# Performance work log

Measured on AMD Instinct MI355X. Metric: run time of the kernel, lower is better.

The kernel has to match this reference:

```python
import jax, jax.numpy as jnp
import numpy as np

H = 12          # trees_num / n_heads
D_WEIGHT = 0.1  # opt['d_weight']
NEG = -1e9


def setup_inputs() -> dict:
    key = jax.random.key(0)
    ks = jax.random.split(key, 6)
    B, N, D = 8, 512, 768
    inp = {}
    inp["input"] = jax.random.normal(ks[0], (B, N, D), dtype=jnp.float32)
    inp["src_mask"] = jax.random.randint(ks[1], (B, 1, N), 0, 2).astype(jnp.int32)
    inp["dep_emb"] = jax.random.normal(ks[2], (B, N, N), dtype=jnp.float32)
    s = 1.0 / np.sqrt(D)
    inp["Wq"] = jax.random.normal(ks[3], (D, D), dtype=jnp.float32) * s
    inp["bq"] = jnp.zeros((D,), dtype=jnp.float32)
    inp["Wk"] = jax.random.normal(ks[4], (D, D), dtype=jnp.float32) * s
    inp["bk"] = jnp.zeros((D,), dtype=jnp.float32)
    return inp


def reference(input, src_mask, dep_emb, Wq, bq, Wk, bk):
    B, N, D = input.shape
    dk = D // H
    # Q/K projections -> [B, H, N, dk]
    q = (input @ Wq + bq).reshape(B, N, H, dk).transpose(0, 2, 1, 3)
    k = (input @ Wk + bk).reshape(B, N, H, dk).transpose(0, 2, 1, 3)
    # scaled scores [B, H, N, N]
    scores = jnp.einsum("bhqd,bhkd->bhqk", q, k) / jnp.sqrt(jnp.asarray(dk, input.dtype))
    # blend with dependency bias: dep_emb [B,N,N] -> [B,1,N,N]
    scores = (1.0 - D_WEIGHT) * scores + D_WEIGHT * dep_emb[:, None, :, :]
    # mask: src_mask [B,1,N] -> [B,1,1,N]; masked_fill(mask==0, -1e9)
    scores = jnp.where(src_mask[:, None, :, :] == 0, NEG, scores)
    p_attn = jax.nn.softmax(scores, axis=-1)  # [B, H, N, N]
    # original returns list of per-head [B,N,N]; full tensor is equivalent
    return p_attn
```

## Files before the change

### kernel.cpp

```cpp
#include <hip/hip_runtime.h>


typedef _Float16 f16;
typedef _Float16 f16x4 __attribute__((ext_vector_type(4)));
typedef _Float16 f16x8 __attribute__((ext_vector_type(8)));
typedef float    f32x4 __attribute__((ext_vector_type(4)));

#define NTOK   512
#define DMODEL 768
#define BATCH  8
#define NHEAD  12
#define NEGV   (-1e9f)

__global__ __launch_bounds__(256)
void convert_x(const float* __restrict__ X, f16* __restrict__ Xh) {
    const size_t i = ((size_t)blockIdx.x * 256 + threadIdx.x) * 4;
    float4 v = *(const float4*)&X[i];
    f16x4 h = { (f16)v.x, (f16)v.y, (f16)v.z, (f16)v.w };
    *(f16x4*)&Xh[i] = h;
}

__global__ __launch_bounds__(256)
void transpose_w(const float* __restrict__ Wq, const float* __restrict__ Wk,
                 f16* __restrict__ Wt) {
    __shared__ float tile[32][33];
    const int kb = blockIdx.x * 32;
    const int nb = blockIdx.y * 32;
    const float* __restrict__ W = (nb < 768) ? Wq : Wk;
    const int nc = (nb < 768) ? nb : nb - 768;
    const int tx = threadIdx.x, ty = threadIdx.y;
    #pragma unroll
    for (int i = 0; i < 4; ++i)
        tile[ty + i*8][tx] = W[(size_t)(kb + ty + i*8) * DMODEL + nc + tx];
    __syncthreads();
    #pragma unroll
    for (int i = 0; i < 4; ++i)
        Wt[(size_t)(nb + ty + i*8) * DMODEL + kb + tx] = (f16)tile[tx][ty + i*8];
}

__global__ __launch_bounds__(64)
void proj_mfma(const f16* __restrict__ Xh, const f16* __restrict__ Wt,
               const float* __restrict__ bq, const float* __restrict__ bk,
               f16* __restrict__ QK) {
    const int m0 = blockIdx.x * 64;
    const int n0 = blockIdx.y * 64;
    const int l = threadIdx.x;
    const int l15 = l & 15, quad = l >> 4;

    f32x4 acc[4][4];
    #pragma unroll
    for (int i = 0; i < 4; ++i)
        #pragma unroll
        for (int j = 0; j < 4; ++j) acc[i][j] = (f32x4){0.f, 0.f, 0.f, 0.f};

    const f16* __restrict__ Ab = Xh + (size_t)(m0 + l15) * DMODEL + quad * 8;
    const f16* __restrict__ Bb = Wt + (size_t)(n0 + l15) * DMODEL + quad * 8;

    for (int ks = 0; ks < DMODEL / 32; ++ks) {
        f16x8 a[4], b[4];
        #pragma unroll
        for (int mi = 0; mi < 4; ++mi)
            a[mi] = *(const f16x8*)(Ab + (size_t)mi * 16 * DMODEL + ks * 32);
        #pragma unroll
        for (int ni = 0; ni < 4; ++ni)
            b[ni] = *(const f16x8*)(Bb + (size_t)ni * 16 * DMODEL + ks * 32);
        #pragma unroll
        for (int mi = 0; mi < 4; ++mi)
            #pragma unroll
            for (int ni = 0; ni < 4; ++ni)
                acc[mi][ni] = __builtin_amdgcn_mfma_f32_16x16x32_f16(
                    a[mi], b[ni], acc[mi][ni], 0, 0, 0);
    }

    const float* __restrict__ bias = (n0 < 768) ? (bq + n0) : (bk + n0 - 768);
    #pragma unroll
    for (int ni = 0; ni < 4; ++ni) {
        const float bv = bias[ni * 16 + l15];
        const int col = n0 + ni * 16 + l15;
        #pragma unroll
        for (int mi = 0; mi < 4; ++mi) {
            #pragma unroll
            for (int r = 0; r < 4; ++r) {
                const int row = m0 + mi * 16 + quad * 4 + r;
                QK[(size_t)row * 1536 + col] = (f16)(acc[mi][ni][r] + bv);
            }
        }
    }
}

__global__ __launch_bounds__(64)
void attn_mfma(const f16* __restrict__ QK, const float* __restrict__ dep,
               const int* __restrict__ mask, float* __restrict__ out) {
    const int qt = blockIdx.x, h = blockIdx.y, b = blockIdx.z;
    const int l = threadIdx.x;
    const int l15 = l & 15, quad = l >> 4;
    const int q0 = qt * 16;

    f32x4 acc[32];
    #pragma unroll
    for (int t = 0; t < 32; ++t) acc[t] = (f32x4){0.f, 0.f, 0.f, 0.f};

    const f16* __restrict__ Qb = QK + (size_t)(b * NTOK + q0 + l15) * 1536 + h * 64 + quad * 8;
    const f16* __restrict__ Kb = QK + (size_t)(b * NTOK + l15) * 1536 + 768 + h * 64 + quad * 8;

    #pragma unroll
    for (int ks = 0; ks < 2; ++ks) {
        f16x8 a = *(const f16x8*)(Qb + ks * 32);
        #pragma unroll
        for (int t = 0; t < 32; ++t) {
            f16x8 bf = *(const f16x8*)(Kb + (size_t)t * 16 * 1536 + ks * 32);
            acc[t] = __builtin_amdgcn_mfma_f32_16x16x32_f16(a, bf, acc[t], 0, 0, 0);
        }
    }

    const float SC = (1.0f - 0.1f) / 8.0f;
    const float DW = 0.1f;
    const float* __restrict__ deprow = dep + ((size_t)b * NTOK + q0 + quad * 4) * NTOK;
    const int*   __restrict__ mrow   = mask + b * NTOK;
    #pragma unroll
    for (int t = 0; t < 32; ++t) {
        const int col = t * 16 + l15;
        const int mv = mrow[col];
        #pragma unroll
        for (int r = 0; r < 4; ++r) {
            const float dv = deprow[(size_t)r * NTOK + col];
            const float s = SC * acc[t][r] + DW * dv;
            acc[t][r] = mv ? s : NEGV;
        }
    }

    float rmax[4] = {NEGV, NEGV, NEGV, NEGV};
    #pragma unroll
    for (int t = 0; t < 32; ++t)
        #pragma unroll
        for (int r = 0; r < 4; ++r) rmax[r] = fmaxf(rmax[r], acc[t][r]);
    #pragma unroll
    for (int r = 0; r < 4; ++r) {
        rmax[r] = fmaxf(rmax[r], __shfl_xor(rmax[r], 1));
        rmax[r] = fmaxf(rmax[r], __shfl_xor(rmax[r], 2));
        rmax[r] = fmaxf(rmax[r], __shfl_xor(rmax[r], 4));
        rmax[r] = fmaxf(rmax[r], __shfl_xor(rmax[r], 8));
    }
    float rsum[4] = {0.f, 0.f, 0.f, 0.f};
    #pragma unroll
    for (int t = 0; t < 32; ++t)
        #pragma unroll
        for (int r = 0; r < 4; ++r) {
            const float e = __expf(acc[t][r] - rmax[r]);
            acc[t][r] = e;
            rsum[r] += e;
        }
    #pragma unroll
    for (int r = 0; r < 4; ++r) {
        rsum[r] += __shfl_xor(rsum[r], 1);
        rsum[r] += __shfl_xor(rsum[r], 2);
        rsum[r] += __shfl_xor(rsum[r], 4);
        rsum[r] += __shfl_xor(rsum[r], 8);
    }
    float inv[4];
    #pragma unroll
    for (int r = 0; r < 4; ++r) inv[r] = 1.0f / rsum[r];

    float* __restrict__ orow = out + ((size_t)((b * NHEAD + h) * NTOK) + q0 + quad * 4) * NTOK;
    #pragma unroll
    for (int t = 0; t < 32; ++t)
        #pragma unroll
        for (int r = 0; r < 4; ++r)
            orow[(size_t)r * NTOK + t * 16 + l15] = acc[t][r] * inv[r];
}

extern "C" void kernel_launch(void* const* d_in, const int* in_sizes, int n_in,
                              void* d_out, int out_size, void* d_ws, size_t ws_size,
                              hipStream_t stream) {
    const float* X    = (const float*)d_in[0];
    const int*   mask = (const int*)  d_in[1];
    const float* dep  = (const float*)d_in[2];
    const float* Wq   = (const float*)d_in[3];
    const float* bq   = (const float*)d_in[4];
    const float* Wk   = (const float*)d_in[5];
    const float* bk   = (const float*)d_in[6];
    float* out = (float*)d_out;

    f16* Xh = (f16*)d_ws;
    f16* Wt = Xh + (size_t)BATCH * NTOK * DMODEL;
    f16* QK = Wt + (size_t)1536 * DMODEL;

    convert_x<<<dim3((BATCH * NTOK * DMODEL) / (256 * 4)), 256, 0, stream>>>(X, Xh);
    transpose_w<<<dim3(DMODEL / 32, 1536 / 32), dim3(32, 8), 0, stream>>>(Wq, Wk, Wt);
    proj_mfma<<<dim3((BATCH * NTOK) / 64, 1536 / 64), 64, 0, stream>>>(Xh, Wt, bq, bk, QK);
    attn_mfma<<<dim3(NTOK / 16, NHEAD, BATCH), 64, 0, stream>>>(QK, dep, mask, out);
}
```

Before: 206.9 us.

## Stage per-head K tile in LDS shared by four waves; merge prep kernels

The attention kernel now uses 256-thread blocks covering 64 query rows. Each block loads the head's full K slice (512x64 f16, padded rows) into shared memory once, and all four waves reuse it, so K is no longer re-read from global memory for every 16-row tile. Separately, the X conversion and weight transpose are merged into one launch to save a kernel launch. The cost is a 72KB LDS allocation per block, which limits occupancy, plus a barrier before any compute can start.

```diff
diff --git a/kernel.cpp b/kernel.cpp
--- a/kernel.cpp
+++ b/kernel.cpp
@@ -11,31 +11,34 @@
 #define BATCH  8
 #define NHEAD  12
 #define NEGV   (-1e9f)
+#define KPAD   72
 
 __global__ __launch_bounds__(256)
-void convert_x(const float* __restrict__ X, f16* __restrict__ Xh) {
-    const size_t i = ((size_t)blockIdx.x * 256 + threadIdx.x) * 4;
-    float4 v = *(const float4*)&X[i];
-    f16x4 h = { (f16)v.x, (f16)v.y, (f16)v.z, (f16)v.w };
-    *(f16x4*)&Xh[i] = h;
-}
-
-__global__ __launch_bounds__(256)
-void transpose_w(const float* __restrict__ Wq, const float* __restrict__ Wk,
+void prep_kernel(const float* __restrict__ X, f16* __restrict__ Xh,
+                 const float* __restrict__ Wq, const float* __restrict__ Wk,
                  f16* __restrict__ Wt) {
-    __shared__ float tile[32][33];
-    const int kb = blockIdx.x * 32;
-    const int nb = blockIdx.y * 32;
-    const float* __restrict__ W = (nb < 768) ? Wq : Wk;
-    const int nc = (nb < 768) ? nb : nb - 768;
-    const int tx = threadIdx.x, ty = threadIdx.y;
-    #pragma unroll
-    for (int i = 0; i < 4; ++i)
-        tile[ty + i*8][tx] = W[(size_t)(kb + ty + i*8) * DMODEL + nc + tx];
-    __syncthreads();
-    #pragma unroll
-    for (int i = 0; i < 4; ++i)
-        Wt[(size_t)(nb + ty + i*8) * DMODEL + kb + tx] = (f16)tile[tx][ty + i*8];
+    const int bx = blockIdx.x;
+    if (bx < 3072) {
+        const size_t i = ((size_t)bx * 256 + threadIdx.x) * 4;
+        float4 v = *(const float4*)&X[i];
+        f16x4 h = { (f16)v.x, (f16)v.y, (f16)v.z, (f16)v.w };
+        *(f16x4*)&Xh[i] = h;
+    } else {
+        __shared__ float tile[32][33];
+        const int id = bx - 3072;
+        const int kb = (id % 24) * 32;
+        const int nb = (id / 24) * 32;
+        const float* __restrict__ W = (nb < 768) ? Wq : Wk;
+        const int nc = (nb < 768) ? nb : nb - 768;
+        const int tx = threadIdx.x & 31, ty = threadIdx.x >> 5;
+        #pragma unroll
+        for (int i = 0; i < 4; ++i)
+            tile[ty + i*8][tx] = W[(size_t)(kb + ty + i*8) * DMODEL + nc + tx];
+        __syncthreads();
+        #pragma unroll
+        for (int i = 0; i < 4; ++i)
+            Wt[(size_t)(nb + ty + i*8) * DMODEL + kb + tx] = (f16)tile[tx][ty + i*8];
+    }
 }
 
 __global__ __launch_bounds__(64)
@@ -78,37 +81,52 @@
         const float bv = bias[ni * 16 + l15];
         const int col = n0 + ni * 16 + l15;
         #pragma unroll
-        for (int mi = 0; mi < 4; ++mi) {
+        for (int mi = 0; mi < 4; ++mi)
             #pragma unroll
             for (int r = 0; r < 4; ++r) {
                 const int row = m0 + mi * 16 + quad * 4 + r;
                 QK[(size_t)row * 1536 + col] = (f16)(acc[mi][ni][r] + bv);
             }
-        }
-    }
-}
-
-__global__ __launch_bounds__(64)
+    }
+}
+
+__global__ __launch_bounds__(256, 2)
 void attn_mfma(const f16* __restrict__ QK, const float* __restrict__ dep,
                const int* __restrict__ mask, float* __restrict__ out) {
     const int qt = blockIdx.x, h = blockIdx.y, b = blockIdx.z;
-    const int l = threadIdx.x;
+    const int tid = threadIdx.x;
+    const int wid = tid >> 6;
+    const int l = tid & 63;
     const int l15 = l & 15, quad = l >> 4;
-    const int q0 = qt * 16;
+    const int q0 = qt * 64 + wid * 16;
+
+    __shared__ f16 Ks[NTOK * KPAD];
+
+    {
+        const f16* __restrict__ Ksrc = QK + (size_t)b * NTOK * 1536 + 768 + h * 64;
+        #pragma unroll
+        for (int c = 0; c < 16; ++c) {
+            const int chunk = tid + c * 256;
+            const int token = chunk >> 3;
+            const int part  = chunk & 7;
+            f16x8 v = *(const f16x8*)(Ksrc + (size_t)token * 1536 + part * 8);
+            *(f16x8*)&Ks[token * KPAD + part * 8] = v;
+        }
+    }
+    __syncthreads();
 
     f32x4 acc[32];
     #pragma unroll
     for (int t = 0; t < 32; ++t) acc[t] = (f32x4){0.f, 0.f, 0.f, 0.f};
 
     const f16* __restrict__ Qb = QK + (size_t)(b * NTOK + q0 + l15) * 1536 + h * 64 + quad * 8;
-    const f16* __restrict__ Kb = QK + (size_t)(b * NTOK + l15) * 1536 + 768 + h * 64 + quad * 8;
 
     #pragma unroll
     for (int ks = 0; ks < 2; ++ks) {
         f16x8 a = *(const f16x8*)(Qb + ks * 32);
         #pragma unroll
         for (int t = 0; t < 32; ++t) {
-            f16x8 bf = *(const f16x8*)(Kb + (size_t)t * 16 * 1536 + ks * 32);
+            f16x8 bf = *(const f16x8*)&Ks[(t * 16 + l15) * KPAD + ks * 32 + quad * 8];
             acc[t] = __builtin_amdgcn_mfma_f32_16x16x32_f16(a, bf, acc[t], 0, 0, 0);
         }
     }
@@ -185,8 +203,7 @@
     f16* Wt = Xh + (size_t)BATCH * NTOK * DMODEL;
     f16* QK = Wt + (size_t)1536 * DMODEL;
 
-    convert_x<<<dim3((BATCH * NTOK * DMODEL) / (256 * 4)), 256, 0, stream>>>(X, Xh);
-    transpose_w<<<dim3(DMODEL / 32, 1536 / 32), dim3(32, 8), 0, stream>>>(Wq, Wk, Wt);
+    prep_kernel<<<dim3(3072 + 1152), 256, 0, stream>>>(X, Xh, Wq, Wk, Wt);
     proj_mfma<<<dim3((BATCH * NTOK) / 64, 1536 / 64), 64, 0, stream>>>(Xh, Wt, bq, bk, QK);
-    attn_mfma<<<dim3(NTOK / 16, NHEAD, BATCH), 64, 0, stream>>>(QK, dep, mask, out);
-}
+    attn_mfma<<<dim3(NTOK / 64, NHEAD, BATCH), 256, 0, stream>>>(QK, dep, mask, out);
+}
```

After: 191.5 us. 7.4% less time.
